# Optimization experiments

Hardware: AMD Instinct MI355X
Metric: run time of the kernel (lower is better)

The kernel has to match this reference:

```python
import jax, jax.numpy as jnp
import numpy as np

NUM_FEATURES = 256
NUM_PIDS = 5554          # must equal hardcoded FocalLoss ignore_index
NUM_CQ = 50000
N_ROIS = 2048
OIM_SCALAR = 30.0
IGNORE_INDEX = 5554
ALPHA = 1.0
GAMMA = 2.0


def _l2norm(x):
    return x / jnp.linalg.norm(x, axis=-1, keepdims=True)


def setup_inputs() -> dict:
    key = jax.random.key(0)
    k1, k2, k3, k4, k5 = jax.random.split(key, 5)
    inputs = _l2norm(jax.random.normal(k1, (N_ROIS, NUM_FEATURES), jnp.float32))
    # targets >= 1 so label = targets-1 >= 0 (the inds filter is all-True -> static shapes)
    # targets == NUM_PIDS+1 -> label == NUM_PIDS == ignore_index (unlabeled, ignored in loss)
    targets = jax.random.randint(k2, (N_ROIS,), 1, NUM_PIDS + 2, dtype=jnp.int64)
    ious = jax.random.uniform(k3, (N_ROIS,), jnp.float32)
    lut = _l2norm(jax.random.normal(k4, (NUM_PIDS, NUM_FEATURES), jnp.float32))
    cq = _l2norm(jax.random.normal(k5, (NUM_CQ, NUM_FEATURES), jnp.float32))
    return {"inputs": inputs, "lut": lut, "cq": cq, "targets": targets, "ious": ious}


def _focal_loss(logits, labels):
    # F.cross_entropy(reduction='none', ignore_index=IGNORE_INDEX) then
    # focal = alpha * (1-pt)^gamma * ce, mean over ALL samples (ignored -> 0).
    logp = jax.nn.log_softmax(logits, axis=-1)                       # [N, C]
    ce = -jnp.take_along_axis(logp, labels[:, None], axis=1)[:, 0]   # [N]
    ce = jnp.where(labels == IGNORE_INDEX, 0.0, ce)
    pt = jnp.exp(-ce)
    return jnp.mean(ALPHA * (1.0 - pt) ** GAMMA * ce)


def reference(inputs, lut, cq, targets, ious):
    # targets = cat(roi_label); label = targets - 1; inds all True by construction.
    label = targets - 1
    # LOIM forward: logits against labeled LUT and unlabeled circular queue.
    table = jnp.concatenate([lut, cq], axis=0)          # [P+Q, D]
    projected = OIM_SCALAR * (inputs @ table.T)         # [N, P+Q]
    loss_oim = _focal_loss(projected, label)
    return loss_oim, inputs, label
```

## Files before the change

kernel.cpp:

```cpp
#include <hip/hip_runtime.h>
#include <hip/hip_bf16.h>


#define NFEAT 256
#define NROIS 2048
#define NPIDS 5554
#define NCLS 55554
#define NCHUNKS 3473
#define NCLSP (NCHUNKS * 16)
#define S2F 43.280851226668906f
#define LN2F 0.6931471805599453f
#define LOFF 524289

typedef float f32x4 __attribute__((ext_vector_type(4)));
typedef short bf16x8 __attribute__((ext_vector_type(8)));
typedef unsigned short u16x8 __attribute__((ext_vector_type(8)));

#if __has_builtin(__builtin_amdgcn_exp2f)
#define EXP2(x) __builtin_amdgcn_exp2f(x)
#else
#define EXP2(x) exp2f(x)
#endif

__device__ __forceinline__ short bfb(float x) {
    return __builtin_bit_cast(short, __float2bfloat16(x));
}

__device__ __forceinline__ void gll16(const void* g, void* l) {
    __builtin_amdgcn_global_load_lds(
        (const __attribute__((address_space(1))) void*)g,
        (__attribute__((address_space(3))) void*)l, 16, 0, 0);
}

__global__ __launch_bounds__(256) void preprocess(
        const float* __restrict__ inputs, const float* __restrict__ lut,
        const float* __restrict__ cq, const int* __restrict__ cand0,
        const int* __restrict__ cand1, unsigned short* __restrict__ tb,
        unsigned short* __restrict__ ab, int* __restrict__ lab,
        float* __restrict__ S, float* __restrict__ f, const int useTB) {
    const int tid = threadIdx.x;
    const int bx = blockIdx.x;

    if (bx == 0) {
        __shared__ int smode;
        __shared__ const int* sT;
        if (tid == 0) {
            const int* T = cand0;
            const unsigned u0 = (unsigned)cand0[0];
            const float f0 = __builtin_bit_cast(float, cand0[0]);
            const bool oki = (u0 >= 1u && u0 <= 6000u);
            const bool okf = (f0 >= 1.0f && f0 <= 6000.0f);
            if (!oki && !okf) T = cand1;
            int mode = 0;
            const unsigned tu0 = (unsigned)T[0];
            const float tf0 = __builtin_bit_cast(float, T[0]);
            if (tu0 >= 1u && tu0 <= 6000u) mode = ((T[1] | T[3] | T[5] | T[7]) == 0) ? 1 : 0;
            else if (tf0 >= 1.0f && tf0 <= 6000.0f) mode = 2;
            smode = mode; sT = T;
        }
        __syncthreads();
        const int mode = smode;
        const int* T = sT;
        for (int j = tid; j < NROIS; j += 256) {
            int tv;
            if (mode == 1)      tv = T[2 * j];
            else if (mode == 2) tv = (int)__builtin_bit_cast(float, T[j]);
            else                tv = T[j];
            const int lv = tv - 1;
            lab[j] = lv;
            f[LOFF + j] = __bfloat162float(__float2bfloat16((float)lv));
        }
        for (int j = tid; j < NROIS + 8; j += 256) S[j] = 0.0f;
    }

    if (bx < 512) {
        const int i = bx * 256 + tid;
        const float4 v = *reinterpret_cast<const float4*>(inputs + (size_t)i * 4);
        float* o = f + 1 + (size_t)i * 4;
        o[0] = v.x; o[1] = v.y; o[2] = v.z; o[3] = v.w;
        if (useTB) {
            ushort4 u;
            u.x = (unsigned short)bfb(v.x); u.y = (unsigned short)bfb(v.y);
            u.z = (unsigned short)bfb(v.z); u.w = (unsigned short)bfb(v.w);
            *reinterpret_cast<ushort4*>(ab + (size_t)i * 4) = u;
        }
    }

    if (useTB) {
        const size_t LUTN = (size_t)NPIDS * NFEAT;
        const size_t TOT  = (size_t)NCLS * NFEAT;
        const size_t TOTP = (size_t)NCLSP * NFEAT;
        const size_t stride = (size_t)gridDim.x * 256 * 8;
        for (size_t e = ((size_t)bx * 256 + tid) * 8; e < TOTP; e += stride) {
            u16x8 o = {0, 0, 0, 0, 0, 0, 0, 0};
            if (e < TOT) {
                const float* sp = (e < LUTN) ? (lut + e) : (cq + (e - LUTN));
                const float4 a = *reinterpret_cast<const float4*>(sp);
                const float4 b = *reinterpret_cast<const float4*>(sp + 4);
                o[0] = (unsigned short)bfb(a.x); o[1] = (unsigned short)bfb(a.y);
                o[2] = (unsigned short)bfb(a.z); o[3] = (unsigned short)bfb(a.w);
                o[4] = (unsigned short)bfb(b.x); o[5] = (unsigned short)bfb(b.y);
                o[6] = (unsigned short)bfb(b.z); o[7] = (unsigned short)bfb(b.w);
            }
            *reinterpret_cast<u16x8*>(tb + e) = o;
        }
    }
}

template <bool TB>
__global__ __launch_bounds__(256, 2) void main_gemm3(const float* __restrict__ inputs,
                                                     const unsigned short* __restrict__ tb,
                                                     const unsigned short* __restrict__ ab,
                                                     const float* __restrict__ lut,
                                                     const float* __restrict__ cq,
                                                     float* __restrict__ S) {
    __shared__ short ldsb[3][4096];
    const int tid = threadIdx.x;
    const int lane = tid & 63;
    const int wave = tid >> 6;
    const int cs = blockIdx.x & 63;
    const int rg = blockIdx.x >> 6;
    const int rowbase = rg * 256 + wave * 64;
    const int li = lane & 15;
    const int q = lane >> 4;
    const int xorli = 4 * (li & 7);

    bf16x8 afrag[4][8];
    if constexpr (TB) {
        #pragma unroll
        for (int s = 0; s < 4; s++) {
            const unsigned short* rp = ab + (size_t)(rowbase + s * 16 + li) * NFEAT + q * 8;
            #pragma unroll
            for (int kc = 0; kc < 8; kc++)
                afrag[s][kc] = *reinterpret_cast<const bf16x8*>(rp + kc * 32);
        }
    } else {
        #pragma unroll
        for (int s = 0; s < 4; s++) {
            const float* rp = inputs + (size_t)(rowbase + s * 16 + li) * NFEAT + q * 8;
            #pragma unroll
            for (int kc = 0; kc < 8; kc++) {
                const float4 x0 = *reinterpret_cast<const float4*>(rp + kc * 32);
                const float4 x1 = *reinterpret_cast<const float4*>(rp + kc * 32 + 4);
                bf16x8 a;
                a[0] = bfb(x0.x); a[1] = bfb(x0.y); a[2] = bfb(x0.z); a[3] = bfb(x0.w);
                a[4] = bfb(x1.x); a[5] = bfb(x1.y); a[6] = bfb(x1.z); a[7] = bfb(x1.w);
                afrag[s][kc] = a;
            }
        }
    }

    const int s0 = tid, s1 = tid + 256;
    const int cc0 = s0 >> 5, cc1 = s1 >> 5;
    const int uo0 = ((s0 & 31) ^ (4 * (cc0 & 7))) * 8;
    const int uo1 = ((s1 & 31) ^ (4 * (cc1 & 7))) * 8;

    const int cA = (cs * NCHUNKS) >> 6;
    const int cB = ((cs + 1) * NCHUNKS) >> 6;
    const int NB = cB - cA;

    float sums[4][4] = {{0.f,0.f,0.f,0.f},{0.f,0.f,0.f,0.f},
                        {0.f,0.f,0.f,0.f},{0.f,0.f,0.f,0.f}};
    char* const lbase = (char*)&ldsb[0][0];

    if constexpr (TB) {
        const int ld0 = wave * 1024;
        const int ld1 = 4096 + wave * 1024;
        const unsigned short* p0 = tb + (size_t)(cA * 16 + cc0) * NFEAT + uo0;
        const unsigned short* p1 = tb + (size_t)(cA * 16 + cc1) * NFEAT + uo1;
        int ob0 = 0, ob1 = 8192, ob2 = 16384;

        gll16(p0, lbase + ob0 + ld0);
        gll16(p1, lbase + ob0 + ld1);
        p0 += 16 * NFEAT; p1 += 16 * NFEAT;
        if (NB > 1) {
            gll16(p0, lbase + ob1 + ld0);
            gll16(p1, lbase + ob1 + ld1);
            p0 += 16 * NFEAT; p1 += 16 * NFEAT;
        }

        for (int i = 0; i < NB; ++i) {
            if (i + 1 < NB) asm volatile("s_waitcnt vmcnt(2)\n\ts_barrier" ::: "memory");
            else            asm volatile("s_waitcnt vmcnt(0)\n\ts_barrier" ::: "memory");
            if (i + 2 < NB) {
                gll16(p0, lbase + ob2 + ld0);
                gll16(p1, lbase + ob2 + ld1);
                p0 += 16 * NFEAT; p1 += 16 * NFEAT;
            }
            f32x4 acc[4] = {{0.f,0.f,0.f,0.f},{0.f,0.f,0.f,0.f},
                            {0.f,0.f,0.f,0.f},{0.f,0.f,0.f,0.f}};
            #pragma unroll
            for (int kc = 0; kc < 8; kc++) {
                const int slot = li * 32 + ((q + 4 * kc) ^ xorli);
                const bf16x8 b = *reinterpret_cast<const bf16x8*>(lbase + ob0 + slot * 16);
                acc[0] = __builtin_amdgcn_mfma_f32_16x16x32_bf16(afrag[0][kc], b, acc[0], 0, 0, 0);
                acc[1] = __builtin_amdgcn_mfma_f32_16x16x32_bf16(afrag[1][kc], b, acc[1], 0, 0, 0);
                acc[2] = __builtin_amdgcn_mfma_f32_16x16x32_bf16(afrag[2][kc], b, acc[2], 0, 0, 0);
                acc[3] = __builtin_amdgcn_mfma_f32_16x16x32_bf16(afrag[3][kc], b, acc[3], 0, 0, 0);
            }
            #pragma unroll
            for (int s = 0; s < 4; s++)
                #pragma unroll
                for (int r = 0; r < 4; r++)
                    sums[s][r] += EXP2(S2F * acc[s][r] - S2F);
            const int t = ob0; ob0 = ob1; ob1 = ob2; ob2 = t;
        }
    } else {
        {
            int n0 = cA * 16 + cc0; n0 = n0 < (NCLS - 1) ? n0 : (NCLS - 1);
            int n1 = cA * 16 + cc1; n1 = n1 < (NCLS - 1) ? n1 : (NCLS - 1);
            const float* r0 = ((n0 < NPIDS) ? lut + (size_t)n0 * NFEAT
                                            : cq + (size_t)(n0 - NPIDS) * NFEAT) + uo0;
            const float* r1 = ((n1 < NPIDS) ? lut + (size_t)n1 * NFEAT
                                            : cq + (size_t)(n1 - NPIDS) * NFEAT) + uo1;
            const float4 a0 = *reinterpret_cast<const float4*>(r0);
            const float4 a1 = *reinterpret_cast<const float4*>(r0 + 4);
            const float4 b0 = *reinterpret_cast<const float4*>(r1);
            const float4 b1 = *reinterpret_cast<const float4*>(r1 + 4);
            bf16x8 v0, v1;
            v0[0]=bfb(a0.x); v0[1]=bfb(a0.y); v0[2]=bfb(a0.z); v0[3]=bfb(a0.w);
            v0[4]=bfb(a1.x); v0[5]=bfb(a1.y); v0[6]=bfb(a1.z); v0[7]=bfb(a1.w);
            v1[0]=bfb(b0.x); v1[1]=bfb(b0.y); v1[2]=bfb(b0.z); v1[3]=bfb(b0.w);
            v1[4]=bfb(b1.x); v1[5]=bfb(b1.y); v1[6]=bfb(b1.z); v1[7]=bfb(b1.w);
            *reinterpret_cast<bf16x8*>(&ldsb[0][s0 * 8]) = v0;
            *reinterpret_cast<bf16x8*>(&ldsb[0][s1 * 8]) = v1;
        }
        __syncthreads();
        int cur = 0;
        for (int ci = cA; ci < cB; ++ci) {
            const bool pf = (ci + 1 < cB);
            float4 f0a, f0b, f1a, f1b;
            if (pf) {
                int n0 = (ci + 1) * 16 + cc0; n0 = n0 < (NCLS - 1) ? n0 : (NCLS - 1);
                int n1 = (ci + 1) * 16 + cc1; n1 = n1 < (NCLS - 1) ? n1 : (NCLS - 1);
                const float* r0 = ((n0 < NPIDS) ? lut + (size_t)n0 * NFEAT
                                                : cq + (size_t)(n0 - NPIDS) * NFEAT) + uo0;
                const float* r1 = ((n1 < NPIDS) ? lut + (size_t)n1 * NFEAT
                                                : cq + (size_t)(n1 - NPIDS) * NFEAT) + uo1;
                f0a = *reinterpret_cast<const float4*>(r0);
                f0b = *reinterpret_cast<const float4*>(r0 + 4);
                f1a = *reinterpret_cast<const float4*>(r1);
                f1b = *reinterpret_cast<const float4*>(r1 + 4);
            }
            f32x4 acc[4] = {{0.f,0.f,0.f,0.f},{0.f,0.f,0.f,0.f},
                            {0.f,0.f,0.f,0.f},{0.f,0.f,0.f,0.f}};
            #pragma unroll
            for (int kc = 0; kc < 8; kc++) {
                const int slot = li * 32 + ((q + 4 * kc) ^ xorli);
                const bf16x8 b = *reinterpret_cast<const bf16x8*>(&ldsb[cur][slot * 8]);
                acc[0] = __builtin_amdgcn_mfma_f32_16x16x32_bf16(afrag[0][kc], b, acc[0], 0, 0, 0);
                acc[1] = __builtin_amdgcn_mfma_f32_16x16x32_bf16(afrag[1][kc], b, acc[1], 0, 0, 0);
                acc[2] = __builtin_amdgcn_mfma_f32_16x16x32_bf16(afrag[2][kc], b, acc[2], 0, 0, 0);
                acc[3] = __builtin_amdgcn_mfma_f32_16x16x32_bf16(afrag[3][kc], b, acc[3], 0, 0, 0);
            }
            const float valid = ((ci * 16 + li) < NCLS) ? 1.0f : 0.0f;
            #pragma unroll
            for (int s = 0; s < 4; s++)
                #pragma unroll
                for (int r = 0; r < 4; r++)
                    sums[s][r] += valid * EXP2(S2F * (acc[s][r] - 1.0f));
            if (pf) {
                bf16x8 p0, p1;
                p0[0]=bfb(f0a.x); p0[1]=bfb(f0a.y); p0[2]=bfb(f0a.z); p0[3]=bfb(f0a.w);
                p0[4]=bfb(f0b.x); p0[5]=bfb(f0b.y); p0[6]=bfb(f0b.z); p0[7]=bfb(f0b.w);
                p1[0]=bfb(f1a.x); p1[1]=bfb(f1a.y); p1[2]=bfb(f1a.z); p1[3]=bfb(f1a.w);
                p1[4]=bfb(f1b.x); p1[5]=bfb(f1b.y); p1[6]=bfb(f1b.z); p1[7]=bfb(f1b.w);
                *reinterpret_cast<bf16x8*>(&ldsb[cur ^ 1][s0 * 8]) = p0;
                *reinterpret_cast<bf16x8*>(&ldsb[cur ^ 1][s1 * 8]) = p1;
            }
            __syncthreads();
            cur ^= 1;
        }
    }

    #pragma unroll
    for (int s = 0; s < 4; s++)
        #pragma unroll
        for (int r = 0; r < 4; r++) {
            float v = sums[s][r];
            v += __shfl_xor(v, 1); v += __shfl_xor(v, 2);
            v += __shfl_xor(v, 4); v += __shfl_xor(v, 8);
            sums[s][r] = v;
        }
    if (li == 0) {
        #pragma unroll
        for (int s = 0; s < 4; s++)
            #pragma unroll
            for (int r = 0; r < 4; r++)
                atomicAdd(&S[rowbase + s * 16 + q * 4 + r], sums[s][r]);
    }
}

__global__ __launch_bounds__(256) void focal_final(const float* __restrict__ inputs,
                                                   const float* __restrict__ lut,
                                                   const int* __restrict__ lab,
                                                   const float* __restrict__ S,
                                                   float* __restrict__ loss_acc,
                                                   unsigned int* __restrict__ cnt,
                                                   float* __restrict__ f) {
    const int wave = threadIdx.x >> 6;
    const int lane = threadIdx.x & 63;
    const int row = blockIdx.x * 4 + wave;
    const int label = lab[row];
    const bool valid = (label >= 0 && label < NPIDS);
    const int lr = valid ? label : 0;
    const float4 a = *reinterpret_cast<const float4*>(inputs + (size_t)row * NFEAT + lane * 4);
    const float4 b = *reinterpret_cast<const float4*>(lut + (size_t)lr * NFEAT + lane * 4);
    float v = a.x * b.x + a.y * b.y + a.z * b.z + a.w * b.w;
    #pragma unroll
    for (int m = 1; m < 64; m <<= 1) v += __shfl_xor(v, m);

    __shared__ float red[4];
    if (lane == 0) {
        float fo = 0.0f;
        if (valid) {
            const float l2 = v * S2F;
            const float lse2 = S2F + log2f(S[row]);
            float ce = fmaxf((lse2 - l2) * LN2F, 0.0f);
            const float pt = EXP2(l2 - lse2);
            const float om = 1.0f - pt;
            fo = om * om * ce;
        }
        red[wave] = fo;
    }
    __syncthreads();
    if (threadIdx.x == 0) {
        atomicAdd(loss_acc, red[0] + red[1] + red[2] + red[3]);
        __threadfence();
        const unsigned done = atomicAdd(cnt, 1u) + 1u;
        if (done == gridDim.x) {
            const float tot = atomicAdd(loss_acc, 0.0f);
            f[0] = tot * (1.0f / NROIS);
        }
    }
}

extern "C" void kernel_launch(void* const* d_in, const int* in_sizes, int n_in,
                              void* d_out, int out_size, void* d_ws, size_t ws_size,
                              hipStream_t stream) {
    const float* inputs = (const float*)d_in[0];
    const float* lut    = (const float*)d_in[1];
    const float* cq     = (const float*)d_in[2];
    const int*   cand0  = (const int*)d_in[3];
    const int*   cand1  = (const int*)((n_in > 4) ? d_in[4] : d_in[3]);
    float* f = (float*)d_out;

    const size_t TBB = (size_t)NCLSP * NFEAT * 2;
    const size_t ABB = (size_t)NROIS * NFEAT * 2;
    char* ws = (char*)d_ws;
    const bool useTB = ws_size >= TBB + ABB + 32768;

    unsigned short* tb = useTB ? (unsigned short*)ws : nullptr;
    unsigned short* ab = useTB ? (unsigned short*)(ws + TBB) : nullptr;
    float* S = useTB ? (float*)(ws + TBB + ABB) : (float*)ws;
    float* loss_acc    = S + NROIS;
    unsigned int* cnt  = (unsigned int*)(S + NROIS + 1);
    int* lab           = (int*)(S + NROIS + 8);

    preprocess<<<useTB ? 4096 : 512, 256, 0, stream>>>(inputs, lut, cq, cand0, cand1,
                                                       tb, ab, lab, S, f, useTB ? 1 : 0);
    if (useTB) main_gemm3<true><<<512, 256, 0, stream>>>(inputs, tb, ab, lut, cq, S);
    else       main_gemm3<false><<<512, 256, 0, stream>>>(inputs, tb, ab, lut, cq, S);
    focal_final<<<512, 256, 0, stream>>>(inputs, lut, lab, S, loss_acc, cnt, f);
}
```

Before: 176.7 us.

## Widen class tiles to 32 per stage with batched LDS reads and MFMA priority

```diff
diff --git a/kernel.cpp b/kernel.cpp
--- a/kernel.cpp
+++ b/kernel.cpp
@@ -7,7 +7,8 @@
 #define NPIDS 5554
 #define NCLS 55554
 #define NCHUNKS 3473
-#define NCLSP (NCHUNKS * 16)
+#define NCH32 1737
+#define NCLSP (NCH32 * 32)
 #define S2F 43.280851226668906f
 #define LN2F 0.6931471805599453f
 #define LOFF 524289
@@ -108,13 +109,13 @@
 }
 
 template <bool TB>
-__global__ __launch_bounds__(256, 2) void main_gemm3(const float* __restrict__ inputs,
+__global__ __launch_bounds__(256, 2) void main_gemm4(const float* __restrict__ inputs,
                                                      const unsigned short* __restrict__ tb,
                                                      const unsigned short* __restrict__ ab,
                                                      const float* __restrict__ lut,
                                                      const float* __restrict__ cq,
                                                      float* __restrict__ S) {
-    __shared__ short ldsb[3][4096];
+    __shared__ short ldsb[3][8192];
     const int tid = threadIdx.x;
     const int lane = tid & 63;
     const int wave = tid >> 6;
@@ -150,62 +151,76 @@
         }
     }
 
-    const int s0 = tid, s1 = tid + 256;
-    const int cc0 = s0 >> 5, cc1 = s1 >> 5;
-    const int uo0 = ((s0 & 31) ^ (4 * (cc0 & 7))) * 8;
-    const int uo1 = ((s1 & 31) ^ (4 * (cc1 & 7))) * 8;
-
-    const int cA = (cs * NCHUNKS) >> 6;
-    const int cB = ((cs + 1) * NCHUNKS) >> 6;
-    const int NB = cB - cA;
-
     float sums[4][4] = {{0.f,0.f,0.f,0.f},{0.f,0.f,0.f,0.f},
                         {0.f,0.f,0.f,0.f},{0.f,0.f,0.f,0.f}};
     char* const lbase = (char*)&ldsb[0][0];
 
     if constexpr (TB) {
-        const int ld0 = wave * 1024;
-        const int ld1 = 4096 + wave * 1024;
-        const unsigned short* p0 = tb + (size_t)(cA * 16 + cc0) * NFEAT + uo0;
-        const unsigned short* p1 = tb + (size_t)(cA * 16 + cc1) * NFEAT + uo1;
-        int ob0 = 0, ob1 = 8192, ob2 = 16384;
-
-        gll16(p0, lbase + ob0 + ld0);
-        gll16(p1, lbase + ob0 + ld1);
-        p0 += 16 * NFEAT; p1 += 16 * NFEAT;
+        const int cc0 = tid >> 5;
+        const int uo = ((tid & 31) ^ (4 * (cc0 & 7))) * 8;
+        const int ldd = wave * 1024;
+        const int cA = (cs * NCH32) >> 6;
+        const int cB = ((cs + 1) * NCH32) >> 6;
+        const int NB = cB - cA;
+        const unsigned short* psrc = tb + (size_t)(cA * 32 + cc0) * NFEAT + uo;
+        int ob0 = 0, ob1 = 16384, ob2 = 32768;
+
+        #pragma unroll
+        for (int k = 0; k < 4; k++)
+            gll16(psrc + (size_t)(8 * k) * NFEAT, lbase + ob0 + ldd + k * 4096);
+        psrc += (size_t)32 * NFEAT;
         if (NB > 1) {
-            gll16(p0, lbase + ob1 + ld0);
-            gll16(p1, lbase + ob1 + ld1);
-            p0 += 16 * NFEAT; p1 += 16 * NFEAT;
+            #pragma unroll
+            for (int k = 0; k < 4; k++)
+                gll16(psrc + (size_t)(8 * k) * NFEAT, lbase + ob1 + ldd + k * 4096);
+            psrc += (size_t)32 * NFEAT;
         }
 
         for (int i = 0; i < NB; ++i) {
-            if (i + 1 < NB) asm volatile("s_waitcnt vmcnt(2)\n\ts_barrier" ::: "memory");
+            if (i + 1 < NB) asm volatile("s_waitcnt vmcnt(4)\n\ts_barrier" ::: "memory");
             else            asm volatile("s_waitcnt vmcnt(0)\n\ts_barrier" ::: "memory");
             if (i + 2 < NB) {
-                gll16(p0, lbase + ob2 + ld0);
-                gll16(p1, lbase + ob2 + ld1);
-                p0 += 16 * NFEAT; p1 += 16 * NFEAT;
-            }
-            f32x4 acc[4] = {{0.f,0.f,0.f,0.f},{0.f,0.f,0.f,0.f},
-                            {0.f,0.f,0.f,0.f},{0.f,0.f,0.f,0.f}};
-            #pragma unroll
-            for (int kc = 0; kc < 8; kc++) {
-                const int slot = li * 32 + ((q + 4 * kc) ^ xorli);
-                const bf16x8 b = *reinterpret_cast<const bf16x8*>(lbase + ob0 + slot * 16);
-                acc[0] = __builtin_amdgcn_mfma_f32_16x16x32_bf16(afrag[0][kc], b, acc[0], 0, 0, 0);
-                acc[1] = __builtin_amdgcn_mfma_f32_16x16x32_bf16(afrag[1][kc], b, acc[1], 0, 0, 0);
-                acc[2] = __builtin_amdgcn_mfma_f32_16x16x32_bf16(afrag[2][kc], b, acc[2], 0, 0, 0);
-                acc[3] = __builtin_amdgcn_mfma_f32_16x16x32_bf16(afrag[3][kc], b, acc[3], 0, 0, 0);
-            }
-            #pragma unroll
-            for (int s = 0; s < 4; s++)
-                #pragma unroll
-                for (int r = 0; r < 4; r++)
-                    sums[s][r] += EXP2(S2F * acc[s][r] - S2F);
+                #pragma unroll
+                for (int k = 0; k < 4; k++)
+                    gll16(psrc + (size_t)(8 * k) * NFEAT, lbase + ob2 + ldd + k * 4096);
+                psrc += (size_t)32 * NFEAT;
+            }
+            #pragma unroll
+            for (int h = 0; h < 2; h++) {
+                const int cc = h * 16 + li;
+                bf16x8 bfr[8];
+                #pragma unroll
+                for (int kc = 0; kc < 8; kc++) {
+                    const int slot = cc * 32 + ((q + 4 * kc) ^ xorli);
+                    bfr[kc] = *reinterpret_cast<const bf16x8*>(lbase + ob0 + slot * 16);
+                }
+                f32x4 acc[4] = {{0.f,0.f,0.f,0.f},{0.f,0.f,0.f,0.f},
+                                {0.f,0.f,0.f,0.f},{0.f,0.f,0.f,0.f}};
+                __builtin_amdgcn_s_setprio(1);
+                #pragma unroll
+                for (int kc = 0; kc < 8; kc++) {
+                    acc[0] = __builtin_amdgcn_mfma_f32_16x16x32_bf16(afrag[0][kc], bfr[kc], acc[0], 0, 0, 0);
+                    acc[1] = __builtin_amdgcn_mfma_f32_16x16x32_bf16(afrag[1][kc], bfr[kc], acc[1], 0, 0, 0);
+                    acc[2] = __builtin_amdgcn_mfma_f32_16x16x32_bf16(afrag[2][kc], bfr[kc], acc[2], 0, 0, 0);
+                    acc[3] = __builtin_amdgcn_mfma_f32_16x16x32_bf16(afrag[3][kc], bfr[kc], acc[3], 0, 0, 0);
+                }
+                __builtin_amdgcn_s_setprio(0);
+                #pragma unroll
+                for (int s = 0; s < 4; s++)
+                    #pragma unroll
+                    for (int r = 0; r < 4; r++)
+                        sums[s][r] += EXP2(S2F * acc[s][r] - S2F);
+            }
             const int t = ob0; ob0 = ob1; ob1 = ob2; ob2 = t;
         }
     } else {
+        short* fb = (short*)lbase;
+        const int s0 = tid, s1 = tid + 256;
+        const int cc0 = s0 >> 5, cc1 = s1 >> 5;
+        const int uo0 = ((s0 & 31) ^ (4 * (cc0 & 7))) * 8;
+        const int uo1 = ((s1 & 31) ^ (4 * (cc1 & 7))) * 8;
+        const int cA = (cs * NCHUNKS) >> 6;
+        const int cB = ((cs + 1) * NCHUNKS) >> 6;
         {
             int n0 = cA * 16 + cc0; n0 = n0 < (NCLS - 1) ? n0 : (NCLS - 1);
             int n1 = cA * 16 + cc1; n1 = n1 < (NCLS - 1) ? n1 : (NCLS - 1);
@@ -222,8 +237,8 @@
             v0[4]=bfb(a1.x); v0[5]=bfb(a1.y); v0[6]=bfb(a1.z); v0[7]=bfb(a1.w);
             v1[0]=bfb(b0.x); v1[1]=bfb(b0.y); v1[2]=bfb(b0.z); v1[3]=bfb(b0.w);
             v1[4]=bfb(b1.x); v1[5]=bfb(b1.y); v1[6]=bfb(b1.z); v1[7]=bfb(b1.w);
-            *reinterpret_cast<bf16x8*>(&ldsb[0][s0 * 8]) = v0;
-            *reinterpret_cast<bf16x8*>(&ldsb[0][s1 * 8]) = v1;
+            *reinterpret_cast<bf16x8*>(&fb[s0 * 8]) = v0;
+            *reinterpret_cast<bf16x8*>(&fb[s1 * 8]) = v1;
         }
         __syncthreads();
         int cur = 0;
@@ -247,7 +262,7 @@
             #pragma unroll
             for (int kc = 0; kc < 8; kc++) {
                 const int slot = li * 32 + ((q + 4 * kc) ^ xorli);
-                const bf16x8 b = *reinterpret_cast<const bf16x8*>(&ldsb[cur][slot * 8]);
+                const bf16x8 b = *reinterpret_cast<const bf16x8*>(&fb[cur * 4096 + slot * 8]);
                 acc[0] = __builtin_amdgcn_mfma_f32_16x16x32_bf16(afrag[0][kc], b, acc[0], 0, 0, 0);
                 acc[1] = __builtin_amdgcn_mfma_f32_16x16x32_bf16(afrag[1][kc], b, acc[1], 0, 0, 0);
                 acc[2] = __builtin_amdgcn_mfma_f32_16x16x32_bf16(afrag[2][kc], b, acc[2], 0, 0, 0);
@@ -265,8 +280,8 @@
                 p0[4]=bfb(f0b.x); p0[5]=bfb(f0b.y); p0[6]=bfb(f0b.z); p0[7]=bfb(f0b.w);
                 p1[0]=bfb(f1a.x); p1[1]=bfb(f1a.y); p1[2]=bfb(f1a.z); p1[3]=bfb(f1a.w);
                 p1[4]=bfb(f1b.x); p1[5]=bfb(f1b.y); p1[6]=bfb(f1b.z); p1[7]=bfb(f1b.w);
-                *reinterpret_cast<bf16x8*>(&ldsb[cur ^ 1][s0 * 8]) = p0;
-                *reinterpret_cast<bf16x8*>(&ldsb[cur ^ 1][s1 * 8]) = p1;
+                *reinterpret_cast<bf16x8*>(&fb[(cur ^ 1) * 4096 + s0 * 8]) = p0;
+                *reinterpret_cast<bf16x8*>(&fb[(cur ^ 1) * 4096 + s1 * 8]) = p1;
             }
             __syncthreads();
             cur ^= 1;
@@ -359,7 +374,7 @@
 
     preprocess<<<useTB ? 4096 : 512, 256, 0, stream>>>(inputs, lut, cq, cand0, cand1,
                                                        tb, ab, lab, S, f, useTB ? 1 : 0);
-    if (useTB) main_gemm3<true><<<512, 256, 0, stream>>>(inputs, tb, ab, lut, cq, S);
-    else       main_gemm3<false><<<512, 256, 0, stream>>>(inputs, tb, ab, lut, cq, S);
+    if (useTB) main_gemm4<true><<<512, 256, 0, stream>>>(inputs, tb, ab, lut, cq, S);
+    else       main_gemm4<false><<<512, 256, 0, stream>>>(inputs, tb, ab, lut, cq, S);
     focal_final<<<512, 256, 0, stream>>>(inputs, lut, lab, S, loss_acc, cnt, f);
 }
```

Result: faster. 171.5 us (median of 2 runs) (-2.9%).
